# Optimization experiments

Measured on AMD Instinct MI355X. Metric: run time of the kernel, lower is better.

Reference implementation:

```python
import jax, jax.numpy as jnp
import numpy as np

B, NL, NH, CL, CH = 16, 4096, 1024, 128, 256
MLP = [256, 256]
BN_EPS = 1e-5


def setup_inputs() -> dict:
    key = jax.random.key(0)
    ks = jax.random.split(key, 8)
    inp = {
        "xyz_low": jax.random.normal(ks[0], (B, NL, 3), dtype=jnp.float32),
        "xyz_high": jax.random.normal(ks[1], (B, NH, 3), dtype=jnp.float32),
        "feat_low": jax.random.normal(ks[2], (B, CL, NL), dtype=jnp.float32),
        "feat_high": jax.random.normal(ks[3], (B, CH, NH), dtype=jnp.float32),
    }
    last = CL + CH
    for i, oc in enumerate(MLP):
        inp[f"W{i}"] = jax.random.normal(ks[4 + i], (oc, last), dtype=jnp.float32) * (1.0 / np.sqrt(last))
        inp[f"b{i}"] = jnp.zeros((oc,), dtype=jnp.float32)
        inp[f"gamma{i}"] = jnp.ones((oc,), dtype=jnp.float32)
        inp[f"beta{i}"] = jnp.zeros((oc,), dtype=jnp.float32)
        last = oc
    return inp


def _bn_relu(x, gamma, beta):
    # BatchNorm1d in training mode: batch stats over (B, N) per channel (biased var)
    mean = x.mean(axis=(0, 2), keepdims=True)
    var = ((x - mean) ** 2).mean(axis=(0, 2), keepdims=True)
    y = gamma[None, :, None] * (x - mean) * jax.lax.rsqrt(var + BN_EPS) + beta[None, :, None]
    return jax.nn.relu(y)


def _forward(xyz_low, xyz_high, feat_low, feat_high,
             W0, b0, gamma0, beta0, W1, b1, gamma1, beta1):
    # pairwise euclidean distances (B, NL, NH)
    d2 = (jnp.sum(xyz_low ** 2, -1)[:, :, None]
          + jnp.sum(xyz_high ** 2, -1)[:, None, :]
          - 2.0 * jnp.einsum('bnd,bmd->bnm', xyz_low, xyz_high))
    d = jnp.sqrt(jnp.maximum(d2, 0.0))
    # 3 nearest neighbours (smallest distances)
    _, idx = jax.lax.top_k(-d, 3)                       # (B, NL, 3)
    dist = jnp.maximum(jnp.take_along_axis(d, idx, axis=-1), 1e-8)
    w = 1.0 / dist
    w = w / w.sum(axis=-1, keepdims=True)               # (B, NL, 3)
    fT = jnp.swapaxes(feat_high, 1, 2)                  # (B, NH, CH)
    neigh = jax.vmap(lambda f, i: f[i])(fT, idx)        # (B, NL, 3, CH)
    f_interp = jnp.einsum('bnk,bnkc->bcn', w, neigh)    # (B, CH, NL)
    x = jnp.concatenate([f_interp, feat_low], axis=1)   # (B, CL+CH, NL)
    # 1x1 Conv -> BN -> ReLU stack
    x = _bn_relu(jnp.einsum('bcn,oc->bon', x, W0) + b0[None, :, None], gamma0, beta0)
    x = _bn_relu(jnp.einsum('bcn,oc->bon', x, W1) + b1[None, :, None], gamma1, beta1)
    return x


def reference(xyz_low, xyz_high, feat_low, feat_high,
              W0, b0, gamma0, beta0, W1, b1, gamma1, beta1):
    return _forward(xyz_low, xyz_high, feat_low, feat_high,
                    W0, b0, gamma0, beta0, W1, b1, gamma1, beta1)
```

## Files before the change

kernel.cpp:

```cpp
#include <hip/hip_runtime.h>
#include <math.h>

#define BB 16
#define NL 4096
#define NH 1024
#define CL 128
#define CHH 256
#define K0 384
#define K1 256
#define CO 256
#define BN_EPS 1e-5f

typedef __attribute__((ext_vector_type(8))) short bfrag;
typedef __attribute__((ext_vector_type(4))) float f32x4;
typedef __attribute__((ext_vector_type(4))) unsigned short ushort4b;

__device__ inline unsigned short f2bf(float f) {
    unsigned int u = __builtin_bit_cast(unsigned int, f);
    u += 0x7fffu + ((u >> 16) & 1u);
    return (unsigned short)(u >> 16);
}
__device__ inline float bf2f(unsigned short h) {
    unsigned int u = ((unsigned int)h) << 16;
    return __builtin_bit_cast(float, u);
}

__global__ __launch_bounds__(256) void k_setup(const float* __restrict__ W0s,
                                               unsigned short* __restrict__ Wb0,
                                               const float* __restrict__ W1s,
                                               unsigned short* __restrict__ Wb1,
                                               const float* __restrict__ xyzh,
                                               float4* __restrict__ cand4) {
    int i = blockIdx.x * 256 + threadIdx.x;
    if (i < CO * K0) Wb0[i] = f2bf(W0s[i]);
    if (i < CO * K1) Wb1[i] = f2bf(W1s[i]);
    if (i < BB * NH) {
        float x = xyzh[3 * i], y = xyzh[3 * i + 1], z = xyzh[3 * i + 2];
        float ss = __fadd_rn(__fadd_rn(__fmul_rn(x, x), __fmul_rn(y, y)),
                             __fmul_rn(z, z));
        cand4[i] = make_float4(x, y, z, ss);
    }
}

__global__ __launch_bounds__(256) void k_transpose_fh(const float* __restrict__ fh,
                                                      unsigned short* __restrict__ fT) {
    __shared__ float s[32][33];
    int b = blockIdx.z;
    int c0 = blockIdx.y * 32;
    int m0 = blockIdx.x * 32;
    int tx = threadIdx.x % 32, ty = threadIdx.x / 32;
    const float* src = fh + (size_t)b * CHH * NH;
    unsigned short* dst = fT + (size_t)b * NH * CHH;
#pragma unroll
    for (int j = 0; j < 4; j++)
        s[ty + 8 * j][tx] = src[(size_t)(c0 + ty + 8 * j) * NH + m0 + tx];
    __syncthreads();
    int mi = threadIdx.x >> 3;
    int cp = threadIdx.x & 7;
#pragma unroll
    for (int h = 0; h < 2; h++) {
        int ci = (cp + 8 * h) * 2;
        unsigned int o = (unsigned int)f2bf(s[ci][mi]) |
                         ((unsigned int)f2bf(s[ci + 1][mi]) << 16);
        *(unsigned int*)&dst[(size_t)(m0 + mi) * CHH + c0 + ci] = o;
    }
}

__global__ __launch_bounds__(256) void k_knn(const float* __restrict__ xyzl,
                                             const float4* __restrict__ cand4,
                                             int* __restrict__ idx,
                                             float* __restrict__ wgt) {
    __shared__ float4 cnd[NH];
    __shared__ float tls[4][64][3];
    __shared__ int   ils[4][64][3];

    int b = blockIdx.y;
    for (int p = threadIdx.x; p < NH; p += 256)
        cnd[p] = cand4[(size_t)b * NH + p];
    __syncthreads();

    int lane = threadIdx.x & 63;
    int w = threadIdx.x >> 6;
    int n = blockIdx.x * 64 + lane;

    const float* xl = xyzl + ((size_t)b * NL + n) * 3;
    float l0 = xl[0], l1 = xl[1], l2 = xl[2];
    float a = __fadd_rn(__fadd_rn(__fmul_rn(l0, l0), __fmul_rn(l1, l1)),
                        __fmul_rn(l2, l2));

    float t0 = INFINITY, t1 = INFINITY, t2 = INFINITY;
    int i0 = 0, i1 = 0, i2 = 0;
    int mb = w * 256;
#pragma unroll 8
    for (int j = 0; j < 256; j++) {
        float4 c = cnd[mb + j];
        int m = mb + j;
        float dot = __fadd_rn(__fadd_rn(__fmul_rn(l0, c.x), __fmul_rn(l1, c.y)),
                              __fmul_rn(l2, c.z));
        float dd = __fsub_rn(__fadd_rn(a, c.w), __fmul_rn(2.0f, dot));
        bool c0 = dd < t0, c1 = dd < t1, c2 = dd < t2;
        float nt0 = fminf(dd, t0);
        float nt1 = __builtin_amdgcn_fmed3f(dd, t0, t1);
        float nt2 = __builtin_amdgcn_fmed3f(dd, t1, t2);
        i2 = c1 ? i1 : (c2 ? m : i2);
        i1 = c0 ? i0 : (c1 ? m : i1);
        i0 = c0 ? m : i0;
        t0 = nt0; t1 = nt1; t2 = nt2;
    }
    tls[w][lane][0] = t0; tls[w][lane][1] = t1; tls[w][lane][2] = t2;
    ils[w][lane][0] = i0; ils[w][lane][1] = i1; ils[w][lane][2] = i2;
    __syncthreads();

    if (threadIdx.x < 64) {
        int p = threadIdx.x;
        float u0 = tls[0][p][0], u1 = tls[0][p][1], u2 = tls[0][p][2];
        int   j0 = ils[0][p][0], j1 = ils[0][p][1], j2 = ils[0][p][2];
#pragma unroll
        for (int sg = 1; sg < 4; sg++) {
#pragma unroll
            for (int e = 0; e < 3; e++) {
                float dd = tls[sg][p][e];
                int m = ils[sg][p][e];
                bool c0 = dd < u0, c1 = dd < u1, c2 = dd < u2;
                u2 = c1 ? u1 : (c2 ? dd : u2);
                j2 = c1 ? j1 : (c2 ? m : j2);
                u1 = c0 ? u0 : (c1 ? dd : u1);
                j1 = c0 ? j0 : (c1 ? m : j1);
                u0 = c0 ? dd : u0;
                j0 = c0 ? m : j0;
            }
        }
        u0 = fmaxf(u0, 0.0f); u1 = fmaxf(u1, 0.0f); u2 = fmaxf(u2, 0.0f);
        float d0 = sqrtf(u0), d1 = sqrtf(u1), d2 = sqrtf(u2);
        float w0 = 1.0f / fmaxf(d0, 1e-8f);
        float w1 = 1.0f / fmaxf(d1, 1e-8f);
        float w2 = 1.0f / fmaxf(d2, 1e-8f);
        float wsum = __fadd_rn(__fadd_rn(w0, w1), w2);
        w0 /= wsum; w1 /= wsum; w2 /= wsum;
        int nn = blockIdx.x * 64 + p;
        size_t base = ((size_t)b * NL + nn) * 3;
        idx[base] = j0; idx[base + 1] = j1; idx[base + 2] = j2;
        wgt[base] = w0; wgt[base + 1] = w1; wgt[base + 2] = w2;
    }
}

__global__ __launch_bounds__(256) void k_fl_t(const float* __restrict__ fl,
                                              unsigned short* __restrict__ Xb2) {
    __shared__ unsigned short s[32][68];
    int b = blockIdx.z, c0 = blockIdx.y * 32, n0 = blockIdx.x * 64;
    int tx = threadIdx.x & 63, ty = threadIdx.x >> 6;
    const float* src = fl + ((size_t)b * CL + c0) * NL + n0;
#pragma unroll
    for (int i = 0; i < 8; i++) {
        int c = ty * 8 + i;
        s[c][tx] = f2bf(src[(size_t)c * NL + tx]);
    }
    __syncthreads();
    int n = threadIdx.x >> 2, q = threadIdx.x & 3;
    ushort4b o0, o1;
#pragma unroll
    for (int e = 0; e < 4; e++) o0[e] = s[q * 8 + e][n];
#pragma unroll
    for (int e = 0; e < 4; e++) o1[e] = s[q * 8 + 4 + e][n];
    unsigned short* dst = Xb2 + ((size_t)b * NL + n0 + n) * CL + c0 + q * 8;
    *(ushort4b*)dst = o0;
    *(ushort4b*)(dst + 4) = o1;
}

__device__ inline bfrag bnrelu8(bfrag v, f32x4 s0, f32x4 s1, f32x4 h0, f32x4 h1) {
    bfrag o;
#pragma unroll
    for (int e = 0; e < 4; e++)
        o[e] = (short)f2bf(fmaxf(fmaf(s0[e], bf2f((unsigned short)v[e]), h0[e]), 0.f));
#pragma unroll
    for (int e = 0; e < 4; e++)
        o[4 + e] = (short)f2bf(fmaxf(fmaf(s1[e], bf2f((unsigned short)v[4 + e]), h1[e]), 0.f));
    return o;
}

__device__ inline bfrag interp8(bfrag f0, bfrag f1, bfrag f2,
                                float w0, float w1, float w2) {
    bfrag o;
#pragma unroll
    for (int e = 0; e < 8; e++) {
        float f = __fadd_rn(__fadd_rn(__fmul_rn(w0, bf2f((unsigned short)f0[e])),
                                      __fmul_rn(w1, bf2f((unsigned short)f1[e]))),
                            __fmul_rn(w2, bf2f((unsigned short)f2[e])));
        o[e] = (short)f2bf(f);
    }
    return o;
}

__device__ inline int swz(int r, int cb) {
    return r * 32 + ((cb ^ ((r >> 1) & 3)) << 3);
}

template <int K, bool INTERP, bool BN>
__global__ __launch_bounds__(512) void k_gemmf(const unsigned short* __restrict__ X,
                                               const unsigned short* __restrict__ fT,
                                               const int* __restrict__ idx,
                                               const float* __restrict__ wgt,
                                               const unsigned short* __restrict__ Wb,
                                               const float* __restrict__ bias,
                                               const float* __restrict__ bnsc,
                                               const float* __restrict__ bnsh,
                                               unsigned short* __restrict__ Y,
                                               float* __restrict__ psumT,
                                               float* __restrict__ psqT) {
    __shared__ __align__(16) unsigned short sA[2][256 * 32];
    __shared__ __align__(16) unsigned short sB[2][128 * 32];

    int bt = blockIdx.x;
    int xcd = bt & 7, ii = bt >> 3;
    int b  = xcd * 2 + (ii >> 5);
    int n0 = (ii & 31) * 128;

    int tid = threadIdx.x;
    int lane = tid & 63;
    int wid = tid >> 6;
    int wm = wid >> 1, wn = wid & 1;

    int sr = tid >> 2;
    int scb = tid & 3;
    int swA0 = swz(sr, scb), swA1 = swz(sr + 128, scb);
    int swB = swz(sr, scb);

    const unsigned short* Wt = Wb + scb * 8;
    int nrow = n0 + sr;

    const unsigned short* fTb;
    int ba0 = 0, ba1 = 0, ba2 = 0;
    float iw0 = 0.f, iw1 = 0.f, iw2 = 0.f;
    if (INTERP) {
        size_t ib = ((size_t)b * NL + nrow) * 3;
        ba0 = idx[ib] * CHH; ba1 = idx[ib + 1] * CHH; ba2 = idx[ib + 2] * CHH;
        iw0 = wgt[ib]; iw1 = wgt[ib + 1]; iw2 = wgt[ib + 2];
        fTb = fT + (size_t)b * NH * CHH;
    }
    const unsigned short* Xrow =
        X + ((size_t)b * NL + nrow) * (INTERP ? CL : CO);

    f32x4 acc[4][4] = {};

    auto stageB = [&](int tt, bfrag& r0, bfrag& r1, bfrag& r2) {
        int cg = tt * 32 + scb * 8;
        if (INTERP) {
            if (cg < CHH) {
                r0 = *(const bfrag*)&fTb[ba0 + cg];
                r1 = *(const bfrag*)&fTb[ba1 + cg];
                r2 = *(const bfrag*)&fTb[ba2 + cg];
            } else {
                r0 = *(const bfrag*)&Xrow[cg - CHH];
            }
        } else {
            r0 = *(const bfrag*)&Xrow[cg];
        }
    };
    auto combineB = [&](int tt, bfrag r0, bfrag r1, bfrag r2) -> bfrag {
        int cg = tt * 32 + scb * 8;
        if (INTERP) {
            if (cg < CHH) return interp8(r0, r1, r2, iw0, iw1, iw2);
            return r0;
        }
        if (BN) {
            f32x4 sc0 = *(const f32x4*)&bnsc[cg], sc1 = *(const f32x4*)&bnsc[cg + 4];
            f32x4 sh0 = *(const f32x4*)&bnsh[cg], sh1 = *(const f32x4*)&bnsh[cg + 4];
            return bnrelu8(r0, sc0, sc1, sh0, sh1);
        }
        return r0;
    };

    {
        bfrag a0 = *(const bfrag*)&Wt[(size_t)sr * K];
        bfrag a1 = *(const bfrag*)&Wt[(size_t)(sr + 128) * K];
        bfrag r0, r1, r2;
        stageB(0, r0, r1, r2);
        bfrag bb = combineB(0, r0, r1, r2);
        *(bfrag*)&sA[0][swA0] = a0;
        *(bfrag*)&sA[0][swA1] = a1;
        *(bfrag*)&sB[0][swB] = bb;
    }
    __syncthreads();

    const int nkt = K / 32;
    int cur = 0;
#pragma unroll 2
    for (int tt = 0; tt < nkt; tt++) {
        bfrag na0, na1, r0, r1, r2;
        bool more = (tt + 1 < nkt);
        if (more) {
            int kk = (tt + 1) * 32;
            na0 = *(const bfrag*)&Wt[(size_t)sr * K + kk];
            na1 = *(const bfrag*)&Wt[(size_t)(sr + 128) * K + kk];
            stageB(tt + 1, r0, r1, r2);
        }
        bfrag af[4], bf[4];
#pragma unroll
        for (int mi = 0; mi < 4; mi++) {
            int r = wm * 64 + mi * 16 + (lane & 15);
            af[mi] = *(const bfrag*)&sA[cur][swz(r, lane >> 4)];
        }
#pragma unroll
        for (int ni = 0; ni < 4; ni++) {
            int r = wn * 64 + ni * 16 + (lane & 15);
            bf[ni] = *(const bfrag*)&sB[cur][swz(r, lane >> 4)];
        }
#pragma unroll
        for (int mi = 0; mi < 4; mi++)
#pragma unroll
            for (int ni = 0; ni < 4; ni++)
                acc[mi][ni] = __builtin_amdgcn_mfma_f32_16x16x32_bf16(
                    af[mi], bf[ni], acc[mi][ni], 0, 0, 0);
        if (more) {
            bfrag nb = combineB(tt + 1, r0, r1, r2);
            *(bfrag*)&sA[cur ^ 1][swA0] = na0;
            *(bfrag*)&sA[cur ^ 1][swA1] = na1;
            *(bfrag*)&sB[cur ^ 1][swB] = nb;
            __syncthreads();
            cur ^= 1;
        }
    }

    int col = lane & 15, rg = (lane >> 4) << 2;
    int slot = bt * 2 + wn;
#pragma unroll
    for (int mi = 0; mi < 4; mi++) {
        int m = wm * 64 + mi * 16 + rg;
        f32x4 bv = *(const f32x4*)&bias[m];
        f32x4 sacc = {0.f, 0.f, 0.f, 0.f}, qacc = {0.f, 0.f, 0.f, 0.f};
#pragma unroll
        for (int ni = 0; ni < 4; ni++) {
            int n = n0 + wn * 64 + ni * 16 + col;
            f32x4 c = acc[mi][ni];
            ushort4b o;
#pragma unroll
            for (int j = 0; j < 4; j++) {
                float sv = c[j] + bv[j];
                o[j] = f2bf(sv);
                sacc[j] += sv;
                qacc[j] += sv * sv;
            }
            *(ushort4b*)&Y[((size_t)b * NL + n) * CO + m] = o;
        }
#pragma unroll
        for (int j = 0; j < 4; j++) {
            float s = sacc[j], q = qacc[j];
#pragma unroll
            for (int off = 1; off < 16; off <<= 1) {
                s += __shfl_xor(s, off, 64);
                q += __shfl_xor(q, off, 64);
            }
            if (col == 0) {
                psumT[(size_t)(m + j) * 1024 + slot] = s;
                psqT[(size_t)(m + j) * 1024 + slot] = q;
            }
        }
    }
}

__global__ __launch_bounds__(256) void k_fin(const float* __restrict__ psumT,
                                             const float* __restrict__ psqT,
                                             const float* __restrict__ gamma,
                                             const float* __restrict__ beta,
                                             float* __restrict__ scale,
                                             float* __restrict__ shift) {
    int c = blockIdx.x;
    const float* ps = psumT + (size_t)c * 1024;
    const float* pq = psqT + (size_t)c * 1024;
    float s = 0.f, q = 0.f;
    for (int i = threadIdx.x; i < 1024; i += 256) { s += ps[i]; q += pq[i]; }
#pragma unroll
    for (int off = 1; off < 64; off <<= 1) {
        s += __shfl_xor(s, off, 64);
        q += __shfl_xor(q, off, 64);
    }
    __shared__ float ls[4], lq[4];
    if ((threadIdx.x & 63) == 0) { ls[threadIdx.x >> 6] = s; lq[threadIdx.x >> 6] = q; }
    __syncthreads();
    if (threadIdx.x == 0) {
        float S = ls[0] + ls[1] + ls[2] + ls[3];
        float Q = lq[0] + lq[1] + lq[2] + lq[3];
        float N = (float)(BB * NL);
        float mean = S / N;
        float var = Q / N - mean * mean;
        float sc = gamma[c] / sqrtf(var + BN_EPS);
        scale[c] = sc;
        shift[c] = beta[c] - mean * sc;
    }
}

__global__ __launch_bounds__(256) void k_out(const unsigned short* __restrict__ y1,
                                             const float* __restrict__ scale,
                                             const float* __restrict__ shift,
                                             float* __restrict__ out) {
    __shared__ float s[64][65];
    int b = blockIdx.z, m0 = blockIdx.y * 64, n0 = blockIdx.x * 64;
    int r = threadIdx.x >> 3;
    int mq = (threadIdx.x & 7) * 8;
#pragma unroll
    for (int it = 0; it < 2; it++) {
        int row = r + it * 32;
        bfrag v = *(const bfrag*)&y1[((size_t)b * NL + n0 + row) * CO + m0 + mq];
#pragma unroll
        for (int e = 0; e < 8; e++) {
            int m = mq + e;
            float f = bf2f((unsigned short)v[e]);
            s[m][row] = fmaxf(fmaf(scale[m0 + m], f, shift[m0 + m]), 0.f);
        }
    }
    __syncthreads();
    int m = threadIdx.x >> 2, nb = (threadIdx.x & 3) * 16;
    float* orow = out + ((size_t)b * CO + m0 + m) * NL + n0 + nb;
#pragma unroll
    for (int i = 0; i < 16; i += 4) {
        float4 v = make_float4(s[m][nb + i], s[m][nb + i + 1],
                               s[m][nb + i + 2], s[m][nb + i + 3]);
        *(float4*)&orow[i] = v;
    }
}

extern "C" void kernel_launch(void* const* d_in, const int* in_sizes, int n_in,
                              void* d_out, int out_size, void* d_ws, size_t ws_size,
                              hipStream_t stream) {
    const float* xyz_low   = (const float*)d_in[0];
    const float* xyz_high  = (const float*)d_in[1];
    const float* feat_low  = (const float*)d_in[2];
    const float* feat_high = (const float*)d_in[3];
    const float* W0  = (const float*)d_in[4];
    const float* b0  = (const float*)d_in[5];
    const float* g0  = (const float*)d_in[6];
    const float* be0 = (const float*)d_in[7];
    const float* W1  = (const float*)d_in[8];
    const float* b1  = (const float*)d_in[9];
    const float* g1  = (const float*)d_in[10];
    const float* be1 = (const float*)d_in[11];
    float* out = (float*)d_out;

    char* ws = (char*)d_ws;
    unsigned short* Xb2 = (unsigned short*)ws;
    unsigned short* y0  = (unsigned short*)(ws + ((size_t)16 << 20));
    unsigned short* y1  = (unsigned short*)(ws + ((size_t)48 << 20));
    unsigned short* fT  = (unsigned short*)(ws + ((size_t)48 << 20));
    char* tail          = ws + ((size_t)80 << 20);
    int*    idx   = (int*)tail;
    float*  wgt   = (float*)(tail + 786432);
    float4* cand4 = (float4*)(tail + 2 * 786432);
    unsigned short* Wb0 = (unsigned short*)(tail + 2 * 786432 + 262144);
    unsigned short* Wb1 = Wb0 + CO * K0;
    char* tail2   = (char*)(Wb1 + CO * K1);
    float* psumT0 = (float*)tail2;
    float* psqT0  = psumT0 + 256 * 1024;
    float* psumT1 = psqT0 + 256 * 1024;
    float* psqT1  = psumT1 + 256 * 1024;
    float* prm    = psqT1 + 256 * 1024;
    float* scale0 = prm,        *shift0 = prm + 256;
    float* scale1 = prm + 512,  *shift1 = prm + 768;

    k_setup<<<(CO * K0 + 255) / 256, 256, 0, stream>>>(W0, Wb0, W1, Wb1,
                                                       xyz_high, cand4);
    k_transpose_fh<<<dim3(NH / 32, CHH / 32, BB), 256, 0, stream>>>(feat_high, fT);
    k_knn<<<dim3(NL / 64, BB), 256, 0, stream>>>(xyz_low, cand4, idx, wgt);
    k_fl_t<<<dim3(NL / 64, CL / 32, BB), 256, 0, stream>>>(feat_low, Xb2);

    k_gemmf<K0, true, false><<<512, 512, 0, stream>>>(
        Xb2, fT, idx, wgt, Wb0, b0, nullptr, nullptr, y0, psumT0, psqT0);
    k_fin<<<256, 256, 0, stream>>>(psumT0, psqT0, g0, be0, scale0, shift0);
    k_gemmf<K1, false, true><<<512, 512, 0, stream>>>(
        y0, nullptr, nullptr, nullptr, Wb1, b1, scale0, shift0, y1, psumT1, psqT1);
    k_fin<<<256, 256, 0, stream>>>(psumT1, psqT1, g1, be1, scale1, shift1);
    k_out<<<dim3(NL / 64, CO / 64, BB), 256, 0, stream>>>(y1, scale1, shift1, out);
}
```

Before: 157.7 us.

## Split GEMM output channels across two 256-thread blocks of 128x128 tiles

Changes the fused GEMM kernels from 512-thread blocks that compute all 256 output channels for 128 points to 256-thread blocks that compute 128 channels by 128 points, doubling the grid to 1024 blocks. Each thread now stages two rows of A and two rows of B. The intent is more blocks for occupancy and load balance across CUs, with less LDS per block. The cost is that the B-side gather and interpolation (and the BN+ReLU on the input) run twice per point tile, once in each channel-half block.

```diff
diff --git a/kernel.cpp b/kernel.cpp
--- a/kernel.cpp
+++ b/kernel.cpp
@@ -196,7 +196,7 @@
 }
 
 template <int K, bool INTERP, bool BN>
-__global__ __launch_bounds__(512) void k_gemmf(const unsigned short* __restrict__ X,
+__global__ __launch_bounds__(256) void k_gemmb(const unsigned short* __restrict__ X,
                                                const unsigned short* __restrict__ fT,
                                                const int* __restrict__ idx,
                                                const float* __restrict__ wgt,
@@ -207,13 +207,16 @@
                                                unsigned short* __restrict__ Y,
                                                float* __restrict__ psumT,
                                                float* __restrict__ psqT) {
-    __shared__ __align__(16) unsigned short sA[2][256 * 32];
+    __shared__ __align__(16) unsigned short sA[2][128 * 32];
     __shared__ __align__(16) unsigned short sB[2][128 * 32];
 
-    int bt = blockIdx.x;
-    int xcd = bt & 7, ii = bt >> 3;
-    int b  = xcd * 2 + (ii >> 5);
-    int n0 = (ii & 31) * 128;
+    int t = blockIdx.x;
+    int xcd = t & 7, ii = t >> 3;
+    int m0 = (ii & 1) * 128;
+    int nb = ii >> 1;
+    int n0 = (nb & 31) * 128;
+    int b  = xcd * 2 + (nb >> 5);
+    int pi2 = (b * 32 + (nb & 31)) * 2;
 
     int tid = threadIdx.x;
     int lane = tid & 63;
@@ -222,63 +225,73 @@
 
     int sr = tid >> 2;
     int scb = tid & 3;
-    int swA0 = swz(sr, scb), swA1 = swz(sr + 128, scb);
-    int swB = swz(sr, scb);
-
-    const unsigned short* Wt = Wb + scb * 8;
-    int nrow = n0 + sr;
-
-    const unsigned short* fTb;
-    int ba0 = 0, ba1 = 0, ba2 = 0;
-    float iw0 = 0.f, iw1 = 0.f, iw2 = 0.f;
+    int swA0 = swz(sr, scb), swA1 = swz(sr + 64, scb);
+
+    const unsigned short* Wt = Wb + (size_t)m0 * K + scb * 8;
+
+    const int XS = INTERP ? CL : CO;
+    const unsigned short* Xr0 = X + ((size_t)b * NL + n0 + sr) * XS + scb * 8;
+    const unsigned short* Xr1 = X + ((size_t)b * NL + n0 + sr + 64) * XS + scb * 8;
+
+    const unsigned short* fTb = nullptr;
+    int a00 = 0, a01 = 0, a02 = 0, a10 = 0, a11 = 0, a12 = 0;
+    float w00 = 0, w01 = 0, w02 = 0, w10 = 0, w11 = 0, w12 = 0;
     if (INTERP) {
-        size_t ib = ((size_t)b * NL + nrow) * 3;
-        ba0 = idx[ib] * CHH; ba1 = idx[ib + 1] * CHH; ba2 = idx[ib + 2] * CHH;
-        iw0 = wgt[ib]; iw1 = wgt[ib + 1]; iw2 = wgt[ib + 2];
-        fTb = fT + (size_t)b * NH * CHH;
-    }
-    const unsigned short* Xrow =
-        X + ((size_t)b * NL + nrow) * (INTERP ? CL : CO);
+        fTb = fT + (size_t)b * NH * CHH + scb * 8;
+        size_t ib0 = ((size_t)b * NL + n0 + sr) * 3;
+        size_t ib1 = ((size_t)b * NL + n0 + sr + 64) * 3;
+        a00 = idx[ib0] * CHH; a01 = idx[ib0 + 1] * CHH; a02 = idx[ib0 + 2] * CHH;
+        w00 = wgt[ib0]; w01 = wgt[ib0 + 1]; w02 = wgt[ib0 + 2];
+        a10 = idx[ib1] * CHH; a11 = idx[ib1 + 1] * CHH; a12 = idx[ib1 + 2] * CHH;
+        w10 = wgt[ib1]; w11 = wgt[ib1 + 1]; w12 = wgt[ib1 + 2];
+    }
 
     f32x4 acc[4][4] = {};
-
-    auto stageB = [&](int tt, bfrag& r0, bfrag& r1, bfrag& r2) {
-        int cg = tt * 32 + scb * 8;
+    bfrag r00, r01, r02, r10, r11, r12;
+
+    auto loadB = [&](int kk) {
         if (INTERP) {
-            if (cg < CHH) {
-                r0 = *(const bfrag*)&fTb[ba0 + cg];
-                r1 = *(const bfrag*)&fTb[ba1 + cg];
-                r2 = *(const bfrag*)&fTb[ba2 + cg];
+            if (kk < CHH) {
+                r00 = *(const bfrag*)&fTb[a00 + kk];
+                r01 = *(const bfrag*)&fTb[a01 + kk];
+                r02 = *(const bfrag*)&fTb[a02 + kk];
+                r10 = *(const bfrag*)&fTb[a10 + kk];
+                r11 = *(const bfrag*)&fTb[a11 + kk];
+                r12 = *(const bfrag*)&fTb[a12 + kk];
             } else {
-                r0 = *(const bfrag*)&Xrow[cg - CHH];
+                r00 = *(const bfrag*)&Xr0[kk - CHH];
+                r10 = *(const bfrag*)&Xr1[kk - CHH];
             }
         } else {
-            r0 = *(const bfrag*)&Xrow[cg];
+            r00 = *(const bfrag*)&Xr0[kk];
+            r10 = *(const bfrag*)&Xr1[kk];
         }
     };
-    auto combineB = [&](int tt, bfrag r0, bfrag r1, bfrag r2) -> bfrag {
-        int cg = tt * 32 + scb * 8;
+    auto makeB = [&](int kk, bfrag& o0, bfrag& o1) {
         if (INTERP) {
-            if (cg < CHH) return interp8(r0, r1, r2, iw0, iw1, iw2);
-            return r0;
-        }
-        if (BN) {
+            if (kk < CHH) {
+                o0 = interp8(r00, r01, r02, w00, w01, w02);
+                o1 = interp8(r10, r11, r12, w10, w11, w12);
+            } else { o0 = r00; o1 = r10; }
+        } else if (BN) {
+            int cg = kk + scb * 8;
             f32x4 sc0 = *(const f32x4*)&bnsc[cg], sc1 = *(const f32x4*)&bnsc[cg + 4];
             f32x4 sh0 = *(const f32x4*)&bnsh[cg], sh1 = *(const f32x4*)&bnsh[cg + 4];
-            return bnrelu8(r0, sc0, sc1, sh0, sh1);
-        }
-        return r0;
+            o0 = bnrelu8(r00, sc0, sc1, sh0, sh1);
+            o1 = bnrelu8(r10, sc0, sc1, sh0, sh1);
+        } else { o0 = r00; o1 = r10; }
     };
 
     {
         bfrag a0 = *(const bfrag*)&Wt[(size_t)sr * K];
-        bfrag a1 = *(const bfrag*)&Wt[(size_t)(sr + 128) * K];
-        bfrag r0, r1, r2;
-        stageB(0, r0, r1, r2);
-        bfrag bb = combineB(0, r0, r1, r2);
+        bfrag a1 = *(const bfrag*)&Wt[(size_t)(sr + 64) * K];
+        loadB(0);
+        bfrag b0, b1;
+        makeB(0, b0, b1);
         *(bfrag*)&sA[0][swA0] = a0;
         *(bfrag*)&sA[0][swA1] = a1;
-        *(bfrag*)&sB[0][swB] = bb;
+        *(bfrag*)&sB[0][swA0] = b0;
+        *(bfrag*)&sB[0][swA1] = b1;
     }
     __syncthreads();
 
@@ -286,13 +299,13 @@
     int cur = 0;
 #pragma unroll 2
     for (int tt = 0; tt < nkt; tt++) {
-        bfrag na0, na1, r0, r1, r2;
+        bfrag na0, na1;
         bool more = (tt + 1 < nkt);
         if (more) {
             int kk = (tt + 1) * 32;
             na0 = *(const bfrag*)&Wt[(size_t)sr * K + kk];
-            na1 = *(const bfrag*)&Wt[(size_t)(sr + 128) * K + kk];
-            stageB(tt + 1, r0, r1, r2);
+            na1 = *(const bfrag*)&Wt[(size_t)(sr + 64) * K + kk];
+            loadB(kk);
         }
         bfrag af[4], bf[4];
 #pragma unroll
@@ -312,20 +325,21 @@
                 acc[mi][ni] = __builtin_amdgcn_mfma_f32_16x16x32_bf16(
                     af[mi], bf[ni], acc[mi][ni], 0, 0, 0);
         if (more) {
-            bfrag nb = combineB(tt + 1, r0, r1, r2);
+            bfrag nb0, nb1;
+            makeB((tt + 1) * 32, nb0, nb1);
             *(bfrag*)&sA[cur ^ 1][swA0] = na0;
             *(bfrag*)&sA[cur ^ 1][swA1] = na1;
-            *(bfrag*)&sB[cur ^ 1][swB] = nb;
+            *(bfrag*)&sB[cur ^ 1][swA0] = nb0;
+            *(bfrag*)&sB[cur ^ 1][swA1] = nb1;
             __syncthreads();
             cur ^= 1;
         }
     }
 
     int col = lane & 15, rg = (lane >> 4) << 2;
-    int slot = bt * 2 + wn;
 #pragma unroll
     for (int mi = 0; mi < 4; mi++) {
-        int m = wm * 64 + mi * 16 + rg;
+        int m = m0 + wm * 64 + mi * 16 + rg;
         f32x4 bv = *(const f32x4*)&bias[m];
         f32x4 sacc = {0.f, 0.f, 0.f, 0.f}, qacc = {0.f, 0.f, 0.f, 0.f};
 #pragma unroll
@@ -351,8 +365,8 @@
                 q += __shfl_xor(q, off, 64);
             }
             if (col == 0) {
-                psumT[(size_t)(m + j) * 1024 + slot] = s;
-                psqT[(size_t)(m + j) * 1024 + slot] = q;
+                psumT[(size_t)(m + j) * 1024 + pi2 + wn] = s;
+                psqT[(size_t)(m + j) * 1024 + pi2 + wn] = q;
             }
         }
     }
@@ -462,10 +476,10 @@
     k_knn<<<dim3(NL / 64, BB), 256, 0, stream>>>(xyz_low, cand4, idx, wgt);
     k_fl_t<<<dim3(NL / 64, CL / 32, BB), 256, 0, stream>>>(feat_low, Xb2);
 
-    k_gemmf<K0, true, false><<<512, 512, 0, stream>>>(
+    k_gemmb<K0, true, false><<<1024, 256, 0, stream>>>(
         Xb2, fT, idx, wgt, Wb0, b0, nullptr, nullptr, y0, psumT0, psqT0);
     k_fin<<<256, 256, 0, stream>>>(psumT0, psqT0, g0, be0, scale0, shift0);
-    k_gemmf<K1, false, true><<<512, 512, 0, stream>>>(
+    k_gemmb<K1, false, true><<<1024, 256, 0, stream>>>(
         y0, nullptr, nullptr, nullptr, Wb1, b1, scale0, shift0, y1, psumT1, psqT1);
     k_fin<<<256, 256, 0, stream>>>(psumT1, psqT1, g1, be1, scale1, shift1);
     k_out<<<dim3(NL / 64, CO / 64, BB), 256, 0, stream>>>(y1, scale1, shift1, out);
```

After: 174.8 us. +10.8%, slower.

## Stage full-K activation tile in LDS, stream weights from global into registers

Applied to the files above, without the earlier changes.

Replaces the double-buffered 256x128 GEMM tile with a 256x64 tile per 256-thread block. The block loads the whole K-extent of the activation (or interpolated) tile into padded LDS once, behind a single barrier. Weight fragments are read directly from global memory (L2-resident) into registers and prefetched one k-step ahead. This removes the per-k-step LDS staging of weights and the repeated barriers. The cost is four times as many global weight reads per output, more blocks, and a larger LDS footprint for K=384.

```diff
diff --git a/kernel.cpp b/kernel.cpp
--- a/kernel.cpp
+++ b/kernel.cpp
@@ -191,12 +191,8 @@
     return o;
 }
 
-__device__ inline int swz(int r, int cb) {
-    return r * 32 + ((cb ^ ((r >> 1) & 3)) << 3);
-}
-
 template <int K, bool INTERP, bool BN>
-__global__ __launch_bounds__(512) void k_gemmf(const unsigned short* __restrict__ X,
+__global__ __launch_bounds__(256) void k_gemmt(const unsigned short* __restrict__ X,
                                                const unsigned short* __restrict__ fT,
                                                const int* __restrict__ idx,
                                                const float* __restrict__ wgt,
@@ -207,130 +203,100 @@
                                                unsigned short* __restrict__ Y,
                                                float* __restrict__ psumT,
                                                float* __restrict__ psqT) {
-    __shared__ __align__(16) unsigned short sA[2][256 * 32];
-    __shared__ __align__(16) unsigned short sB[2][128 * 32];
-
-    int bt = blockIdx.x;
-    int xcd = bt & 7, ii = bt >> 3;
-    int b  = xcd * 2 + (ii >> 5);
-    int n0 = (ii & 31) * 128;
+    constexpr int NBLK = K / 8;
+    constexpr int LROW8 = (NBLK + 1) * 8;
+    __shared__ __align__(16) unsigned short sB[64 * LROW8];
+
+    int t = blockIdx.x;
+    int xcd = t & 7, ii = t >> 3;
+    int b  = xcd * 2 + (ii >> 6);
+    int n0 = (ii & 63) * 64;
 
     int tid = threadIdx.x;
     int lane = tid & 63;
     int wid = tid >> 6;
-    int wm = wid >> 1, wn = wid & 1;
-
-    int sr = tid >> 2;
-    int scb = tid & 3;
-    int swA0 = swz(sr, scb), swA1 = swz(sr + 128, scb);
-    int swB = swz(sr, scb);
-
-    const unsigned short* Wt = Wb + scb * 8;
-    int nrow = n0 + sr;
-
-    const unsigned short* fTb;
-    int ba0 = 0, ba1 = 0, ba2 = 0;
-    float iw0 = 0.f, iw1 = 0.f, iw2 = 0.f;
-    if (INTERP) {
-        size_t ib = ((size_t)b * NL + nrow) * 3;
-        ba0 = idx[ib] * CHH; ba1 = idx[ib + 1] * CHH; ba2 = idx[ib + 2] * CHH;
-        iw0 = wgt[ib]; iw1 = wgt[ib + 1]; iw2 = wgt[ib + 2];
-        fTb = fT + (size_t)b * NH * CHH;
-    }
-    const unsigned short* Xrow =
-        X + ((size_t)b * NL + nrow) * (INTERP ? CL : CO);
-
+
+    {
+        int r = tid >> 2, c4 = tid & 3;
+        int nrow = n0 + r;
+        unsigned short* srow = &sB[r * LROW8];
+        if (INTERP) {
+            size_t ib = ((size_t)b * NL + nrow) * 3;
+            int a0 = idx[ib] * CHH, a1 = idx[ib + 1] * CHH, a2 = idx[ib + 2] * CHH;
+            float w0 = wgt[ib], w1 = wgt[ib + 1], w2 = wgt[ib + 2];
+            const unsigned short* fTb = fT + (size_t)b * NH * CHH;
+            const unsigned short* xr = X + ((size_t)b * NL + nrow) * CL;
+#pragma unroll
+            for (int j = 0; j < 8; j++) {
+                int ke = (c4 + 4 * j) * 8;
+                bfrag f0 = *(const bfrag*)&fTb[a0 + ke];
+                bfrag f1 = *(const bfrag*)&fTb[a1 + ke];
+                bfrag f2 = *(const bfrag*)&fTb[a2 + ke];
+                *(bfrag*)&srow[ke] = interp8(f0, f1, f2, w0, w1, w2);
+            }
+#pragma unroll
+            for (int j = 8; j < NBLK / 4; j++) {
+                int ke = (c4 + 4 * j) * 8;
+                *(bfrag*)&srow[ke] = *(const bfrag*)&xr[ke - CHH];
+            }
+        } else {
+            const unsigned short* xr = X + ((size_t)b * NL + nrow) * CO;
+#pragma unroll
+            for (int j = 0; j < NBLK / 4; j++) {
+                int ke = (c4 + 4 * j) * 8;
+                bfrag v = *(const bfrag*)&xr[ke];
+                if (BN) {
+                    f32x4 sc0 = *(const f32x4*)&bnsc[ke], sc1 = *(const f32x4*)&bnsc[ke + 4];
+                    f32x4 sh0 = *(const f32x4*)&bnsh[ke], sh1 = *(const f32x4*)&bnsh[ke + 4];
+                    v = bnrelu8(v, sc0, sc1, sh0, sh1);
+                }
+                *(bfrag*)&srow[ke] = v;
+            }
+        }
+    }
+    __syncthreads();
+
+    int mrow = wid * 64 + (lane & 15);
+    int kcol = (lane >> 4) * 8;
     f32x4 acc[4][4] = {};
 
-    auto stageB = [&](int tt, bfrag& r0, bfrag& r1, bfrag& r2) {
-        int cg = tt * 32 + scb * 8;
-        if (INTERP) {
-            if (cg < CHH) {
-                r0 = *(const bfrag*)&fTb[ba0 + cg];
-                r1 = *(const bfrag*)&fTb[ba1 + cg];
-                r2 = *(const bfrag*)&fTb[ba2 + cg];
-            } else {
-                r0 = *(const bfrag*)&Xrow[cg - CHH];
-            }
-        } else {
-            r0 = *(const bfrag*)&Xrow[cg];
-        }
-    };
-    auto combineB = [&](int tt, bfrag r0, bfrag r1, bfrag r2) -> bfrag {
-        int cg = tt * 32 + scb * 8;
-        if (INTERP) {
-            if (cg < CHH) return interp8(r0, r1, r2, iw0, iw1, iw2);
-            return r0;
-        }
-        if (BN) {
-            f32x4 sc0 = *(const f32x4*)&bnsc[cg], sc1 = *(const f32x4*)&bnsc[cg + 4];
-            f32x4 sh0 = *(const f32x4*)&bnsh[cg], sh1 = *(const f32x4*)&bnsh[cg + 4];
-            return bnrelu8(r0, sc0, sc1, sh0, sh1);
-        }
-        return r0;
-    };
-
-    {
-        bfrag a0 = *(const bfrag*)&Wt[(size_t)sr * K];
-        bfrag a1 = *(const bfrag*)&Wt[(size_t)(sr + 128) * K];
-        bfrag r0, r1, r2;
-        stageB(0, r0, r1, r2);
-        bfrag bb = combineB(0, r0, r1, r2);
-        *(bfrag*)&sA[0][swA0] = a0;
-        *(bfrag*)&sA[0][swA1] = a1;
-        *(bfrag*)&sB[0][swB] = bb;
-    }
-    __syncthreads();
+    bfrag afc[4], afn[4];
+#pragma unroll
+    for (int mi = 0; mi < 4; mi++)
+        afc[mi] = *(const bfrag*)&Wb[(size_t)(mrow + mi * 16) * K + kcol];
 
     const int nkt = K / 32;
-    int cur = 0;
-#pragma unroll 2
+#pragma unroll
     for (int tt = 0; tt < nkt; tt++) {
-        bfrag na0, na1, r0, r1, r2;
-        bool more = (tt + 1 < nkt);
-        if (more) {
-            int kk = (tt + 1) * 32;
-            na0 = *(const bfrag*)&Wt[(size_t)sr * K + kk];
-            na1 = *(const bfrag*)&Wt[(size_t)(sr + 128) * K + kk];
-            stageB(tt + 1, r0, r1, r2);
-        }
-        bfrag af[4], bf[4];
-#pragma unroll
-        for (int mi = 0; mi < 4; mi++) {
-            int r = wm * 64 + mi * 16 + (lane & 15);
-            af[mi] = *(const bfrag*)&sA[cur][swz(r, lane >> 4)];
-        }
-#pragma unroll
-        for (int ni = 0; ni < 4; ni++) {
-            int r = wn * 64 + ni * 16 + (lane & 15);
-            bf[ni] = *(const bfrag*)&sB[cur][swz(r, lane >> 4)];
-        }
+        if (tt + 1 < nkt) {
+            int kb = (tt + 1) * 32 + kcol;
+#pragma unroll
+            for (int mi = 0; mi < 4; mi++)
+                afn[mi] = *(const bfrag*)&Wb[(size_t)(mrow + mi * 16) * K + kb];
+        }
+        bfrag bf[4];
+#pragma unroll
+        for (int ni = 0; ni < 4; ni++)
+            bf[ni] = *(const bfrag*)&sB[(ni * 16 + (lane & 15)) * LROW8 + tt * 32 + kcol];
 #pragma unroll
         for (int mi = 0; mi < 4; mi++)
 #pragma unroll
             for (int ni = 0; ni < 4; ni++)
                 acc[mi][ni] = __builtin_amdgcn_mfma_f32_16x16x32_bf16(
-                    af[mi], bf[ni], acc[mi][ni], 0, 0, 0);
-        if (more) {
-            bfrag nb = combineB(tt + 1, r0, r1, r2);
-            *(bfrag*)&sA[cur ^ 1][swA0] = na0;
-            *(bfrag*)&sA[cur ^ 1][swA1] = na1;
-            *(bfrag*)&sB[cur ^ 1][swB] = nb;
-            __syncthreads();
-            cur ^= 1;
-        }
+                    afc[mi], bf[ni], acc[mi][ni], 0, 0, 0);
+#pragma unroll
+        for (int mi = 0; mi < 4; mi++) afc[mi] = afn[mi];
     }
 
     int col = lane & 15, rg = (lane >> 4) << 2;
-    int slot = bt * 2 + wn;
 #pragma unroll
     for (int mi = 0; mi < 4; mi++) {
-        int m = wm * 64 + mi * 16 + rg;
+        int m = wid * 64 + mi * 16 + rg;
         f32x4 bv = *(const f32x4*)&bias[m];
         f32x4 sacc = {0.f, 0.f, 0.f, 0.f}, qacc = {0.f, 0.f, 0.f, 0.f};
 #pragma unroll
         for (int ni = 0; ni < 4; ni++) {
-            int n = n0 + wn * 64 + ni * 16 + col;
+            int n = n0 + ni * 16 + col;
             f32x4 c = acc[mi][ni];
             ushort4b o;
 #pragma unroll
@@ -351,8 +317,8 @@
                 q += __shfl_xor(q, off, 64);
             }
             if (col == 0) {
-                psumT[(size_t)(m + j) * 1024 + slot] = s;
-                psqT[(size_t)(m + j) * 1024 + slot] = q;
+                psumT[(size_t)(m + j) * 1024 + t] = s;
+                psqT[(size_t)(m + j) * 1024 + t] = q;
             }
         }
     }
@@ -462,10 +428,10 @@
     k_knn<<<dim3(NL / 64, BB), 256, 0, stream>>>(xyz_low, cand4, idx, wgt);
     k_fl_t<<<dim3(NL / 64, CL / 32, BB), 256, 0, stream>>>(feat_low, Xb2);
 
-    k_gemmf<K0, true, false><<<512, 512, 0, stream>>>(
+    k_gemmt<K0, true, false><<<1024, 256, 0, stream>>>(
         Xb2, fT, idx, wgt, Wb0, b0, nullptr, nullptr, y0, psumT0, psqT0);
     k_fin<<<256, 256, 0, stream>>>(psumT0, psqT0, g0, be0, scale0, shift0);
-    k_gemmf<K1, false, true><<<512, 512, 0, stream>>>(
+    k_gemmt<K1, false, true><<<1024, 256, 0, stream>>>(
         y0, nullptr, nullptr, nullptr, Wb1, b1, scale0, shift0, y1, psumT1, psqT1);
     k_fin<<<256, 256, 0, stream>>>(psumT1, psqT1, g1, be1, scale1, shift1);
     k_out<<<dim3(NL / 64, CO / 64, BB), 256, 0, stream>>>(y1, scale1, shift1, out);
```

Result: slower. 171.3 us (+8.6%).
